# Performance work log

Hardware: AMD Instinct MI355X
Metric: run time of the kernel (lower is better)

The kernel has to match this reference:

```python
import jax, jax.numpy as jnp
import numpy as np

N, K = 512, 17
W, H = 48, 64          # heatmap_size = [W, H]
LOSS_WEIGHT = 1.0
EPS = 1e-9


def setup_inputs() -> dict:
    key = jax.random.key(0)
    k1, k2, k3 = jax.random.split(key, 3)
    pred = jax.random.uniform(k1, (N, K, 2), dtype=jnp.float32)           # normalized kpt coords in [0,1)
    sigma = jax.random.uniform(k2, (N, K, 2), dtype=jnp.float32) * 3.0 + 1.0  # realistic gaussian widths [1,4)
    teacher_hm = jax.random.uniform(k3, (N, K, H, W), dtype=jnp.float32)
    target_weight = jnp.ones((N, K, 1), dtype=jnp.float32)                # joints_3d_visible[..., :1]
    return {"pred": pred, "sigma": sigma, "teacher_hm": teacher_hm,
            "target_weight": target_weight}


def reference(pred, sigma, teacher_hm, target_weight):
    # MSRA unbiased encoding (vectorized branch), gaussian_mode='s2'
    mu_x = pred[..., 0] * W                      # [N,K]
    mu_y = pred[..., 1] * H
    sx = sigma[..., 0]
    sy = sigma[..., 1]

    # visibility mask: gaussian bbox must intersect the heatmap
    mask = ((mu_x - 3.0 * sx < W) & (mu_y - 3.0 * sy < H) &
            (mu_x + 3.0 * sx + 1.0 >= 0) & (mu_y + 3.0 * sy + 1.0 >= 0)
            ).astype(jnp.float32)                # [N,K]
    tw = target_weight[..., 0] * mask            # [N,K]

    x = jnp.arange(W, dtype=jnp.float32)         # [W]
    y = jnp.arange(H, dtype=jnp.float32)         # [H]
    dx2 = (x[None, None, None, :] - mu_x[..., None, None]) ** 2 / (sx[..., None, None] ** 2 + EPS)
    dy2 = (y[None, None, :, None] - mu_y[..., None, None]) ** 2 / (sy[..., None, None] ** 2 + EPS)
    g = jnp.exp(-0.5 * (dx2 + dy2))              # [N,K,H,W]
    target = g * mask[..., None, None]

    # JointsMSELoss with use_target_weight: mean over joints of MSE(w*pred, w*gt)
    w = tw[..., None, None]                      # [N,K,1,1]
    loss = jnp.mean((w * (target - teacher_hm)) ** 2) * LOSS_WEIGHT
    return loss
```

## Files before the change

kernel.cpp:

```cpp
#include <hip/hip_runtime.h>

#define NN 512
#define KK 17
#define WW 48
#define HH 64
#define HW (WW * HH)
#define NK (NN * KK)

typedef float fv4 __attribute__((ext_vector_type(4)));


__global__ __launch_bounds__(256) void reg2hm_partial_kernel(
    const float* __restrict__ pred,
    const float* __restrict__ sigma,
    const float* __restrict__ teacher,
    const float* __restrict__ twgt,
    float* __restrict__ ws)
{
    __shared__ fv4   ex4[KK][WW / 4];
    __shared__ float eys[KK][HH];
    __shared__ float sw[KK];
    __shared__ float wave_sums[4];

    const int n   = blockIdx.x;
    const int nk0 = n * KK;
    const int t   = threadIdx.x;

    if (t < KK) {
        const int nk = nk0 + t;
        const float mu_x = pred[nk * 2 + 0] * (float)WW;
        const float mu_y = pred[nk * 2 + 1] * (float)HH;
        const float sx   = sigma[nk * 2 + 0];
        const float sy   = sigma[nk * 2 + 1];
        const bool m = (mu_x - 3.0f * sx < (float)WW) &&
                       (mu_y - 3.0f * sy < (float)HH) &&
                       (mu_x + 3.0f * sx + 1.0f >= 0.0f) &&
                       (mu_y + 3.0f * sy + 1.0f >= 0.0f);
        sw[t] = twgt[nk] * (m ? 1.0f : 0.0f);
    }

    float* exf = (float*)ex4;
    for (int i = t; i < KK * (WW + HH); i += 256) {
        const int item = i / (WW + HH);
        const int r    = i - item * (WW + HH);
        const int nk   = nk0 + item;
        if (r < WW) {
            const float mu = pred[nk * 2 + 0] * (float)WW;
            const float s  = sigma[nk * 2 + 0];
            const float d  = (float)r - mu;
            exf[item * WW + r] = __expf(-d * d * (0.5f / (s * s + 1e-9f)));
        } else {
            const float mu = pred[nk * 2 + 1] * (float)HH;
            const float s  = sigma[nk * 2 + 1];
            const float d  = (float)(r - WW) - mu;
            eys[item][r - WW] = __expf(-d * d * (0.5f / (s * s + 1e-9f)));
        }
    }
    __syncthreads();

    const int i0 = t;
    const int i1 = t + 256;
    const int i2 = t + 512;
    const int h0 = i0 / 12, s0 = i0 - h0 * 12;
    const int h1 = i1 / 12, s1 = i1 - h1 * 12;
    const int h2 = i2 / 12, s2 = i2 - h2 * 12;

    const fv4* tp = (const fv4*)(teacher + (size_t)nk0 * HW);

    fv4 c0 = __builtin_nontemporal_load(tp + i0);
    fv4 c1 = __builtin_nontemporal_load(tp + i1);
    fv4 c2 = __builtin_nontemporal_load(tp + i2);
    float total = 0.0f;
#pragma unroll 1
    for (int item = 0; item < KK; ++item) {
        fv4 n0, n1, n2;
        if (item < KK - 1) {
            const fv4* np_ = tp + (item + 1) * (HW / 4);
            n0 = __builtin_nontemporal_load(np_ + i0);
            n1 = __builtin_nontemporal_load(np_ + i1);
            n2 = __builtin_nontemporal_load(np_ + i2);
        }
        const fv4   e0 = ex4[item][s0];
        const fv4   e1 = ex4[item][s1];
        const fv4   e2 = ex4[item][s2];
        const float y0 = eys[item][h0];
        const float y1 = eys[item][h1];
        const float y2 = eys[item][h2];

        float acc = 0.0f;
        {
            const fv4 d = e0 * y0 - c0;
            acc += d.x * d.x + d.y * d.y + d.z * d.z + d.w * d.w;
        }
        {
            const fv4 d = e1 * y1 - c1;
            acc += d.x * d.x + d.y * d.y + d.z * d.z + d.w * d.w;
        }
        {
            const fv4 d = e2 * y2 - c2;
            acc += d.x * d.x + d.y * d.y + d.z * d.z + d.w * d.w;
        }
        total += sw[item] * sw[item] * acc;
        c0 = n0; c1 = n1; c2 = n2;
    }

#pragma unroll
    for (int off = 32; off > 0; off >>= 1)
        total += __shfl_down(total, off, 64);

    const int wave = t >> 6;
    const int lane = t & 63;
    if (lane == 0) wave_sums[wave] = total;
    __syncthreads();

    if (t == 0)
        ws[n] = wave_sums[0] + wave_sums[1] + wave_sums[2] + wave_sums[3];
}

__global__ __launch_bounds__(256) void reg2hm_final_kernel(
    const float* __restrict__ ws, float* __restrict__ out)
{
    __shared__ float wave_sums[4];
    const int t = threadIdx.x;
    float sum = 0.0f;
    for (int i = t; i < NN; i += 256) sum += ws[i];
#pragma unroll
    for (int off = 32; off > 0; off >>= 1)
        sum += __shfl_down(sum, off, 64);
    const int wave = t >> 6;
    const int lane = t & 63;
    if (lane == 0) wave_sums[wave] = sum;
    __syncthreads();
    if (t == 0) {
        const float total = wave_sums[0] + wave_sums[1] + wave_sums[2] + wave_sums[3];
        out[0] = total * (1.0f / ((float)NN * KK * HW));
    }
}

extern "C" void kernel_launch(void* const* d_in, const int* in_sizes, int n_in,
                              void* d_out, int out_size, void* d_ws, size_t ws_size,
                              hipStream_t stream) {
    const float* pred    = (const float*)d_in[0];
    const float* sigma   = (const float*)d_in[1];
    const float* teacher = (const float*)d_in[2];
    const float* twgt    = (const float*)d_in[3];
    float* out = (float*)d_out;
    float* ws  = (float*)d_ws;

    reg2hm_partial_kernel<<<NN, 256, 0, stream>>>(pred, sigma, teacher, twgt, ws);
    reg2hm_final_kernel<<<1, 256, 0, stream>>>(ws, out);
}
```

Measured before the change: 155.7 us.

## Split each sample's heatmaps into row quarters across blocks with deeper prefetch

Each sample is now handled by four blocks of 192 threads, each owning a quarter of the heatmap rows, where before one block of 256 threads covered all rows. Each thread handles one float4 per joint and keeps three joints of loads in flight as a rotating prefetch pipeline. The aim is more blocks and more memory parallelism on a bandwidth-bound streaming read. The trade-off is that the column Gaussian table and the visibility weights are recomputed in every block.

```diff
diff --git a/kernel.cpp b/kernel.cpp
--- a/kernel.cpp
+++ b/kernel.cpp
@@ -5,12 +5,16 @@
 #define WW 48
 #define HH 64
 #define HW (WW * HH)
-#define NK (NN * KK)
+#define NQ 4
+#define RQ (HH / NQ)
+#define FQ (RQ * (WW / 4))
+#define TPB FQ
+#define GRID (NN * NQ)
 
 typedef float fv4 __attribute__((ext_vector_type(4)));
 
 
-__global__ __launch_bounds__(256) void reg2hm_partial_kernel(
+__global__ __launch_bounds__(TPB, 6) void reg2hm_partial_kernel(
     const float* __restrict__ pred,
     const float* __restrict__ sigma,
     const float* __restrict__ teacher,
@@ -18,11 +22,13 @@
     float* __restrict__ ws)
 {
     __shared__ fv4   ex4[KK][WW / 4];
-    __shared__ float eys[KK][HH];
-    __shared__ float sw[KK];
-    __shared__ float wave_sums[4];
+    __shared__ float eys[KK][RQ];
+    __shared__ float sw2[KK];
+    __shared__ float wave_sums[TPB / 64];
 
-    const int n   = blockIdx.x;
+    const int b   = blockIdx.x;
+    const int n   = b >> 2;
+    const int q   = b & 3;
     const int nk0 = n * KK;
     const int t   = threadIdx.x;
 
@@ -36,13 +42,14 @@
                        (mu_y - 3.0f * sy < (float)HH) &&
                        (mu_x + 3.0f * sx + 1.0f >= 0.0f) &&
                        (mu_y + 3.0f * sy + 1.0f >= 0.0f);
-        sw[t] = twgt[nk] * (m ? 1.0f : 0.0f);
+        const float w = twgt[nk] * (m ? 1.0f : 0.0f);
+        sw2[t] = w * w;
     }
 
     float* exf = (float*)ex4;
-    for (int i = t; i < KK * (WW + HH); i += 256) {
-        const int item = i / (WW + HH);
-        const int r    = i - item * (WW + HH);
+    for (int i = t; i < KK * (WW + RQ); i += TPB) {
+        const int item = i / (WW + RQ);
+        const int r    = i - item * (WW + RQ);
         const int nk   = nk0 + item;
         if (r < WW) {
             const float mu = pred[nk * 2 + 0] * (float)WW;
@@ -50,58 +57,34 @@
             const float d  = (float)r - mu;
             exf[item * WW + r] = __expf(-d * d * (0.5f / (s * s + 1e-9f)));
         } else {
+            const int h    = q * RQ + (r - WW);
             const float mu = pred[nk * 2 + 1] * (float)HH;
             const float s  = sigma[nk * 2 + 1];
-            const float d  = (float)(r - WW) - mu;
+            const float d  = (float)h - mu;
             eys[item][r - WW] = __expf(-d * d * (0.5f / (s * s + 1e-9f)));
         }
     }
     __syncthreads();
 
-    const int i0 = t;
-    const int i1 = t + 256;
-    const int i2 = t + 512;
-    const int h0 = i0 / 12, s0 = i0 - h0 * 12;
-    const int h1 = i1 / 12, s1 = i1 - h1 * 12;
-    const int h2 = i2 / 12, s2 = i2 - h2 * 12;
+    const int hl = t / 12;
+    const int s  = t - hl * 12;
 
-    const fv4* tp = (const fv4*)(teacher + (size_t)nk0 * HW);
+    const fv4* tp = (const fv4*)teacher + (size_t)nk0 * (HW / 4) + q * FQ + t;
 
-    fv4 c0 = __builtin_nontemporal_load(tp + i0);
-    fv4 c1 = __builtin_nontemporal_load(tp + i1);
-    fv4 c2 = __builtin_nontemporal_load(tp + i2);
+    fv4 c0 = __builtin_nontemporal_load(tp + 0 * (HW / 4));
+    fv4 c1 = __builtin_nontemporal_load(tp + 1 * (HW / 4));
+    fv4 c2 = __builtin_nontemporal_load(tp + 2 * (HW / 4));
     float total = 0.0f;
 #pragma unroll 1
     for (int item = 0; item < KK; ++item) {
-        fv4 n0, n1, n2;
-        if (item < KK - 1) {
-            const fv4* np_ = tp + (item + 1) * (HW / 4);
-            n0 = __builtin_nontemporal_load(np_ + i0);
-            n1 = __builtin_nontemporal_load(np_ + i1);
-            n2 = __builtin_nontemporal_load(np_ + i2);
-        }
-        const fv4   e0 = ex4[item][s0];
-        const fv4   e1 = ex4[item][s1];
-        const fv4   e2 = ex4[item][s2];
-        const float y0 = eys[item][h0];
-        const float y1 = eys[item][h1];
-        const float y2 = eys[item][h2];
-
-        float acc = 0.0f;
-        {
-            const fv4 d = e0 * y0 - c0;
-            acc += d.x * d.x + d.y * d.y + d.z * d.z + d.w * d.w;
-        }
-        {
-            const fv4 d = e1 * y1 - c1;
-            acc += d.x * d.x + d.y * d.y + d.z * d.z + d.w * d.w;
-        }
-        {
-            const fv4 d = e2 * y2 - c2;
-            acc += d.x * d.x + d.y * d.y + d.z * d.z + d.w * d.w;
-        }
-        total += sw[item] * sw[item] * acc;
-        c0 = n0; c1 = n1; c2 = n2;
+        fv4 nx = c2;
+        if (item + 3 < KK)
+            nx = __builtin_nontemporal_load(tp + (item + 3) * (HW / 4));
+        const fv4   e = ex4[item][s];
+        const float y = eys[item][hl];
+        const fv4   d = e * y - c0;
+        total += sw2[item] * (d.x * d.x + d.y * d.y + d.z * d.z + d.w * d.w);
+        c0 = c1; c1 = c2; c2 = nx;
     }
 
 #pragma unroll
@@ -114,7 +97,7 @@
     __syncthreads();
 
     if (t == 0)
-        ws[n] = wave_sums[0] + wave_sums[1] + wave_sums[2] + wave_sums[3];
+        ws[b] = wave_sums[0] + wave_sums[1] + wave_sums[2];
 }
 
 __global__ __launch_bounds__(256) void reg2hm_final_kernel(
@@ -123,7 +106,7 @@
     __shared__ float wave_sums[4];
     const int t = threadIdx.x;
     float sum = 0.0f;
-    for (int i = t; i < NN; i += 256) sum += ws[i];
+    for (int i = t; i < GRID; i += 256) sum += ws[i];
 #pragma unroll
     for (int off = 32; off > 0; off >>= 1)
         sum += __shfl_down(sum, off, 64);
@@ -147,6 +130,6 @@
     float* out = (float*)d_out;
     float* ws  = (float*)d_ws;
 
-    reg2hm_partial_kernel<<<NN, 256, 0, stream>>>(pred, sigma, teacher, twgt, ws);
+    reg2hm_partial_kernel<<<GRID, TPB, 0, stream>>>(pred, sigma, teacher, twgt, ws);
     reg2hm_final_kernel<<<1, 256, 0, stream>>>(ws, out);
 }
```

Result: slower. 163.4 us (+4.9%).

## Fuse final reduction via last-block atomic counter and deepen teacher prefetch

Applied to the files above, without the earlier changes.

Merges the separate final-reduction kernel into the partial kernel: each block publishes its partial sum with a release store and increments a global counter, and the block that finishes last sums all partials and writes the loss. This removes a second kernel launch and its dependency gap. The teacher heatmap loads are prefetched two items ahead instead of one, which raises register use to hide more memory latency. The squared weight is also precomputed. The counter is never reset and relies on a modulo check, so it assumes every launch completes all blocks.

```diff
diff --git a/kernel.cpp b/kernel.cpp
--- a/kernel.cpp
+++ b/kernel.cpp
@@ -6,21 +6,26 @@
 #define HH 64
 #define HW (WW * HH)
 #define NK (NN * KK)
+#define TPB 256
 
 typedef float fv4 __attribute__((ext_vector_type(4)));
 
+__device__ unsigned int g_done_counter = 0;
 
-__global__ __launch_bounds__(256) void reg2hm_partial_kernel(
+
+__global__ __launch_bounds__(TPB) void reg2hm_fused_kernel(
     const float* __restrict__ pred,
     const float* __restrict__ sigma,
     const float* __restrict__ teacher,
     const float* __restrict__ twgt,
-    float* __restrict__ ws)
+    float* __restrict__ ws,
+    float* __restrict__ out)
 {
     __shared__ fv4   ex4[KK][WW / 4];
     __shared__ float eys[KK][HH];
-    __shared__ float sw[KK];
+    __shared__ float sw2[KK];
     __shared__ float wave_sums[4];
+    __shared__ int   is_last;
 
     const int n   = blockIdx.x;
     const int nk0 = n * KK;
@@ -36,11 +41,12 @@
                        (mu_y - 3.0f * sy < (float)HH) &&
                        (mu_x + 3.0f * sx + 1.0f >= 0.0f) &&
                        (mu_y + 3.0f * sy + 1.0f >= 0.0f);
-        sw[t] = twgt[nk] * (m ? 1.0f : 0.0f);
+        const float w = twgt[nk] * (m ? 1.0f : 0.0f);
+        sw2[t] = w * w;
     }
 
     float* exf = (float*)ex4;
-    for (int i = t; i < KK * (WW + HH); i += 256) {
+    for (int i = t; i < KK * (WW + HH); i += TPB) {
         const int item = i / (WW + HH);
         const int r    = i - item * (WW + HH);
         const int nk   = nk0 + item;
@@ -70,15 +76,18 @@
     fv4 c0 = __builtin_nontemporal_load(tp + i0);
     fv4 c1 = __builtin_nontemporal_load(tp + i1);
     fv4 c2 = __builtin_nontemporal_load(tp + i2);
+    fv4 n0 = __builtin_nontemporal_load(tp + (HW / 4) + i0);
+    fv4 n1 = __builtin_nontemporal_load(tp + (HW / 4) + i1);
+    fv4 n2 = __builtin_nontemporal_load(tp + (HW / 4) + i2);
     float total = 0.0f;
 #pragma unroll 1
     for (int item = 0; item < KK; ++item) {
-        fv4 n0, n1, n2;
-        if (item < KK - 1) {
-            const fv4* np_ = tp + (item + 1) * (HW / 4);
-            n0 = __builtin_nontemporal_load(np_ + i0);
-            n1 = __builtin_nontemporal_load(np_ + i1);
-            n2 = __builtin_nontemporal_load(np_ + i2);
+        fv4 m0 = n0, m1 = n1, m2 = n2;
+        if (item + 2 < KK) {
+            const fv4* np_ = tp + (item + 2) * (HW / 4);
+            m0 = __builtin_nontemporal_load(np_ + i0);
+            m1 = __builtin_nontemporal_load(np_ + i1);
+            m2 = __builtin_nontemporal_load(np_ + i2);
         }
         const fv4   e0 = ex4[item][s0];
         const fv4   e1 = ex4[item][s1];
@@ -100,8 +109,9 @@
             const fv4 d = e2 * y2 - c2;
             acc += d.x * d.x + d.y * d.y + d.z * d.z + d.w * d.w;
         }
-        total += sw[item] * sw[item] * acc;
+        total += sw2[item] * acc;
         c0 = n0; c1 = n1; c2 = n2;
+        n0 = m0; n1 = m1; n2 = m2;
     }
 
 #pragma unroll
@@ -113,27 +123,31 @@
     if (lane == 0) wave_sums[wave] = total;
     __syncthreads();
 
-    if (t == 0)
-        ws[n] = wave_sums[0] + wave_sums[1] + wave_sums[2] + wave_sums[3];
-}
+    if (t == 0) {
+        const float part = wave_sums[0] + wave_sums[1] + wave_sums[2] + wave_sums[3];
+        __hip_atomic_store(&ws[n], part, __ATOMIC_RELEASE,
+                           __HIP_MEMORY_SCOPE_AGENT);
+        const unsigned old = __hip_atomic_fetch_add(
+            &g_done_counter, 1u, __ATOMIC_ACQ_REL, __HIP_MEMORY_SCOPE_AGENT);
+        is_last = ((old % NN) == (NN - 1)) ? 1 : 0;
+    }
+    __syncthreads();
 
-__global__ __launch_bounds__(256) void reg2hm_final_kernel(
-    const float* __restrict__ ws, float* __restrict__ out)
-{
-    __shared__ float wave_sums[4];
-    const int t = threadIdx.x;
-    float sum = 0.0f;
-    for (int i = t; i < NN; i += 256) sum += ws[i];
+    if (is_last) {
+        float sum = 0.0f;
+        for (int i = t; i < NN; i += TPB)
+            sum += __hip_atomic_load(&ws[i], __ATOMIC_RELAXED,
+                                     __HIP_MEMORY_SCOPE_AGENT);
 #pragma unroll
-    for (int off = 32; off > 0; off >>= 1)
-        sum += __shfl_down(sum, off, 64);
-    const int wave = t >> 6;
-    const int lane = t & 63;
-    if (lane == 0) wave_sums[wave] = sum;
-    __syncthreads();
-    if (t == 0) {
-        const float total = wave_sums[0] + wave_sums[1] + wave_sums[2] + wave_sums[3];
-        out[0] = total * (1.0f / ((float)NN * KK * HW));
+        for (int off = 32; off > 0; off >>= 1)
+            sum += __shfl_down(sum, off, 64);
+        if (lane == 0) wave_sums[wave] = sum;
+        __syncthreads();
+        if (t == 0) {
+            const float tot = wave_sums[0] + wave_sums[1] +
+                              wave_sums[2] + wave_sums[3];
+            out[0] = tot * (1.0f / ((float)NN * KK * HW));
+        }
     }
 }
 
@@ -147,6 +161,5 @@
     float* out = (float*)d_out;
     float* ws  = (float*)d_ws;
 
-    reg2hm_partial_kernel<<<NN, 256, 0, stream>>>(pred, sigma, teacher, twgt, ws);
-    reg2hm_final_kernel<<<1, 256, 0, stream>>>(ws, out);
+    reg2hm_fused_kernel<<<NN, TPB, 0, stream>>>(pred, sigma, teacher, twgt, ws, out);
 }
```

Result: slower. 178.1 us (+14.3%).
